# Performance work log

Measured on AMD Instinct MI355X. Metric: run time of the kernel, lower is better.

Reference implementation:

```python
import jax, jax.numpy as jnp
import numpy as np

R = 64          # plane_resolution
C = 32          # plane_channels
H = 128         # mlp_hidden
FEAT = 3 * C


def _grid_sample_bilinear(plane, coords):
    # plane: [C, R, R]; coords: [M, 2] normalized to [-1, 1], (x->W, y->H)
    # align_corners=True, padding_mode='border'
    r = plane.shape[-1]
    ix = (coords[:, 0] + 1.0) * 0.5 * (r - 1)
    iy = (coords[:, 1] + 1.0) * 0.5 * (r - 1)
    ix = jnp.clip(ix, 0.0, r - 1.0)
    iy = jnp.clip(iy, 0.0, r - 1.0)
    x0 = jnp.floor(ix).astype(jnp.int32)
    y0 = jnp.floor(iy).astype(jnp.int32)
    x1 = jnp.minimum(x0 + 1, r - 1)
    y1 = jnp.minimum(y0 + 1, r - 1)
    wx = ix - x0.astype(ix.dtype)
    wy = iy - y0.astype(iy.dtype)
    v00 = plane[:, y0, x0]  # [C, M]
    v01 = plane[:, y0, x1]
    v10 = plane[:, y1, x0]
    v11 = plane[:, y1, x1]
    out = (v00 * (1 - wx) * (1 - wy) + v01 * wx * (1 - wy)
           + v10 * (1 - wx) * wy + v11 * wx * wy)
    return out.T  # [M, C]


def setup_inputs() -> dict:
    key = jax.random.key(0)
    ks = jax.random.split(key, 12)
    B, N = 4, 262144
    points = jax.random.uniform(ks[0], (B, N, 3), dtype=jnp.float32)  # in [0,1) subset of [-1,1]
    planes = jax.random.normal(ks[1], (3, C, R, R), dtype=jnp.float32) * 0.01
    def lin(k, fan_in, fan_out):
        kw, kb = jax.random.split(k)
        bound = 1.0 / np.sqrt(fan_in)
        W = jax.random.uniform(kw, (fan_out, fan_in), jnp.float32, -bound, bound)
        b = jax.random.uniform(kb, (fan_out,), jnp.float32, -bound, bound)
        return W, b
    dW1, db1 = lin(ks[2], FEAT, H)
    dW2, db2 = lin(ks[3], H, H)
    dW3, db3 = lin(ks[4], H, 1)
    rW1, rb1 = lin(ks[5], FEAT, H)
    rW2, rb2 = lin(ks[6], H, 3)
    return dict(points=points, planes=planes,
                dW1=dW1, db1=db1, dW2=dW2, db2=db2, dW3=dW3, db3=db3,
                rW1=rW1, rb1=rb1, rW2=rW2, rb2=rb2)


def reference(points, planes, dW1, db1, dW2, db2, dW3, db3, rW1, rb1, rW2, rb2):
    B, N, _ = points.shape
    p = points.reshape(B * N, 3)
    x, y, z = p[:, 0], p[:, 1], p[:, 2]
    # coords for xy, xz, yz planes: [3, M, 2]
    coords = jnp.stack([jnp.stack([x, y], -1),
                        jnp.stack([x, z], -1),
                        jnp.stack([y, z], -1)], 0)
    feats = jax.vmap(_grid_sample_bilinear)(planes, coords)  # [3, M, C]
    feat = jnp.concatenate([feats[0], feats[1], feats[2]], axis=-1)  # [M, 3C]
    h = jax.nn.relu(feat @ dW1.T + db1)
    h = jax.nn.relu(h @ dW2.T + db2)
    density = jax.nn.softplus(h @ dW3.T + db3)  # [M, 1]
    r = jax.nn.relu(feat @ rW1.T + rb1)
    rgb = jax.nn.sigmoid(r @ rW2.T + rb2)  # [M, 3]
    return rgb.reshape(B, N, 3), density.reshape(B, N, 1)
```

## Files before the change

kernel.cpp:

```cpp
#include <hip/hip_runtime.h>
#include <hip/hip_bf16.h>
#include <math.h>

#define RR 64
#define CC 32
#define NPTS (4*262144)

typedef __attribute__((ext_vector_type(8))) short short8;
typedef __attribute__((ext_vector_type(4))) float f32x4;
typedef __attribute__((ext_vector_type(4))) unsigned int u32x4;

static __device__ inline ushort f2bf(float x) {
    return __builtin_bit_cast(ushort, __float2bfloat16(x));
}
static __device__ inline uint32_t pk2(float a, float b) {
    return (uint32_t)f2bf(a) | ((uint32_t)f2bf(b) << 16);
}
static __device__ inline float relu(float x) { return fmaxf(x, 0.0f); }


__global__ void prepass(const float* __restrict__ planes,
                        const float* __restrict__ dW1, const float* __restrict__ rW1,
                        const float* __restrict__ dW2,
                        const float* __restrict__ db1, const float* __restrict__ rb1,
                        const float* __restrict__ db2, const float* __restrict__ dW3,
                        const float* __restrict__ rW2,
                        float* __restrict__ ws) {
    int tid = blockIdx.x * blockDim.x + threadIdx.x;
    ushort* W1T = (ushort*)(ws + 393216);
    ushort* W2T = W1T + 24576;
    float*  CWS = ws + 393216 + 20480;

    if (tid < 3 * CC * RR * RR) {
        int x = tid % RR, y = (tid / RR) % RR, ch = (tid / (RR * RR)) % CC, p = tid / (CC * RR * RR);
        ws[((p * RR + y) * RR + x) * CC + ch] = planes[tid];
    }
    if (tid < 24576) {
        int e = tid & 7, l = (tid >> 3) & 63, rem = tid >> 9;
        int p = rem % 3, nt = rem / 3;
        int j = nt * 16 + (l & 15);
        int k = p * 32 + (l >> 4) * 8 + e;
        float v = (j < 128) ? dW1[j * 96 + k] : rW1[(j - 128) * 96 + k];
        W1T[tid] = f2bf(v);
    }
    if (tid < 16384) {
        int e = tid & 7, l = (tid >> 3) & 63, rem = tid >> 9;
        int kt2 = rem & 3, nt2 = rem >> 2;
        int j2 = nt2 * 16 + (l & 15);
        int k = kt2 * 32 + (l >> 4) * 8 + e;
        W2T[tid] = f2bf(dW2[j2 * 128 + k]);
    }
    if (tid < 256) CWS[tid]       = (tid < 128) ? db1[tid] : rb1[tid - 128];
    if (tid < 128) CWS[256 + tid] = db2[tid];
    if (tid < 128) CWS[384 + tid] = dW3[tid];
    if (tid < 384) CWS[512 + tid] = rW2[tid];
}

static __device__ inline short8 sample_frag(const float* __restrict__ P,
                                            int plane_base, float cx, float cy, int g8) {
    float ix = (cx + 1.0f) * 31.5f; ix = fminf(fmaxf(ix, 0.0f), 63.0f);
    float iy = (cy + 1.0f) * 31.5f; iy = fminf(fmaxf(iy, 0.0f), 63.0f);
    int x0 = (int)ix, y0 = (int)iy;
    int x1 = min(x0 + 1, 63), y1 = min(y0 + 1, 63);
    float wx = ix - (float)x0, wy = iy - (float)y0;
    float w00 = (1.0f - wx) * (1.0f - wy), w01 = wx * (1.0f - wy);
    float w10 = (1.0f - wx) * wy,          w11 = wx * wy;
    int b00 = plane_base + (y0 * 64 + x0) * 32 + g8;
    int b01 = plane_base + (y0 * 64 + x1) * 32 + g8;
    int b10 = plane_base + (y1 * 64 + x0) * 32 + g8;
    int b11 = plane_base + (y1 * 64 + x1) * 32 + g8;
    f32x4 a0 = *(const f32x4*)(P + b00), a1 = *(const f32x4*)(P + b00 + 4);
    f32x4 c0 = *(const f32x4*)(P + b01), c1 = *(const f32x4*)(P + b01 + 4);
    f32x4 d0 = *(const f32x4*)(P + b10), d1 = *(const f32x4*)(P + b10 + 4);
    f32x4 e0 = *(const f32x4*)(P + b11), e1 = *(const f32x4*)(P + b11 + 4);
    float f0 = w00 * a0[0] + w01 * c0[0] + w10 * d0[0] + w11 * e0[0];
    float f1 = w00 * a0[1] + w01 * c0[1] + w10 * d0[1] + w11 * e0[1];
    float f2 = w00 * a0[2] + w01 * c0[2] + w10 * d0[2] + w11 * e0[2];
    float f3 = w00 * a0[3] + w01 * c0[3] + w10 * d0[3] + w11 * e0[3];
    float f4 = w00 * a1[0] + w01 * c1[0] + w10 * d1[0] + w11 * e1[0];
    float f5 = w00 * a1[1] + w01 * c1[1] + w10 * d1[1] + w11 * e1[1];
    float f6 = w00 * a1[2] + w01 * c1[2] + w10 * d1[2] + w11 * e1[2];
    float f7 = w00 * a1[3] + w01 * c1[3] + w10 * d1[3] + w11 * e1[3];
    u32x4 uu;
    uu[0] = pk2(f0, f1); uu[1] = pk2(f2, f3);
    uu[2] = pk2(f4, f5); uu[3] = pk2(f6, f7);
    return __builtin_bit_cast(short8, uu);
}

#define MFMA(a, b, c) __builtin_amdgcn_mfma_f32_16x16x32_bf16((a), (b), (c), 0, 0, 0)

__global__ __launch_bounds__(512, 2)
void nerf_mfma(const float* __restrict__ points, const float* __restrict__ ws,
               const float* __restrict__ db3g, const float* __restrict__ rb2g,
               float* __restrict__ rgb_out, float* __restrict__ den_out) {
    __shared__ __align__(16) ushort SB[42752];
    __shared__ __align__(16) ushort Hs[8][32][136];

    const float* P = ws;
    int tid = threadIdx.x;

    {
        const u32x4* src = (const u32x4*)(ws + 393216);
        u32x4* dst = (u32x4*)SB;
        #pragma unroll 2
        for (int j = tid; j < 5344; j += 512) dst[j] = src[j];
    }
    __syncthreads();

    const ushort* W1L = SB;
    const ushort* W2L = SB + 24576;
    const float*  Cl  = (const float*)(SB + 40960);

    int wid = tid >> 6, lane = tid & 63;
    int c = lane & 15, g = lane >> 4;
    int g8 = 8 * g;
    ushort (*H)[136] = Hs[wid];
    int gw = blockIdx.x * 8 + wid;

    float b3 = db3g[0];
    float rb0 = rb2g[0], rb1v = rb2g[1], rb2v = rb2g[2];

    for (int it = 0; it < 2; ++it) {
        int pbase = (gw * 2 + it) * 32;

        int ptA = pbase + c, ptB = pbase + c + 16;
        float xa = points[ptA * 3 + 0], ya = points[ptA * 3 + 1], za = points[ptA * 3 + 2];
        float xb = points[ptB * 3 + 0], yb = points[ptB * 3 + 1], zb = points[ptB * 3 + 2];
        short8 bfA0 = sample_frag(P, 0,      xa, ya, g8);
        short8 bfA1 = sample_frag(P, 131072, xa, za, g8);
        short8 bfA2 = sample_frag(P, 262144, ya, za, g8);
        short8 bfB0 = sample_frag(P, 0,      xb, yb, g8);
        short8 bfB1 = sample_frag(P, 131072, xb, zb, g8);
        short8 bfB2 = sample_frag(P, 262144, yb, zb, g8);

        #pragma unroll 4
        for (int nt = 0; nt < 8; ++nt) {
            const ushort* wp = W1L + nt * 1536 + lane * 8;
            short8 a0 = *(const short8*)(wp);
            short8 a1 = *(const short8*)(wp + 512);
            short8 a2 = *(const short8*)(wp + 1024);
            f32x4 accA = {0.f,0.f,0.f,0.f}, accB = {0.f,0.f,0.f,0.f};
            accA = MFMA(a0, bfA0, accA); accB = MFMA(a0, bfB0, accB);
            accA = MFMA(a1, bfA1, accA); accB = MFMA(a1, bfB1, accB);
            accA = MFMA(a2, bfA2, accA); accB = MFMA(a2, bfB2, accB);
            f32x4 bb = *(const f32x4*)(Cl + nt * 16 + 4 * g);
            uint2 wA, wB;
            wA.x = pk2(relu(accA[0] + bb[0]), relu(accA[1] + bb[1]));
            wA.y = pk2(relu(accA[2] + bb[2]), relu(accA[3] + bb[3]));
            wB.x = pk2(relu(accB[0] + bb[0]), relu(accB[1] + bb[1]));
            wB.y = pk2(relu(accB[2] + bb[2]), relu(accB[3] + bb[3]));
            *(uint2*)(&H[c][16 * nt + 4 * g])      = wA;
            *(uint2*)(&H[c + 16][16 * nt + 4 * g]) = wB;
        }

        float racc0A = 0.f, racc0B = 0.f, racc1A = 0.f, racc1B = 0.f, racc2A = 0.f, racc2B = 0.f;
        #pragma unroll 4
        for (int nt = 8; nt < 16; ++nt) {
            const ushort* wp = W1L + nt * 1536 + lane * 8;
            short8 a0 = *(const short8*)(wp);
            short8 a1 = *(const short8*)(wp + 512);
            short8 a2 = *(const short8*)(wp + 1024);
            f32x4 accA = {0.f,0.f,0.f,0.f}, accB = {0.f,0.f,0.f,0.f};
            accA = MFMA(a0, bfA0, accA); accB = MFMA(a0, bfB0, accB);
            accA = MFMA(a1, bfA1, accA); accB = MFMA(a1, bfB1, accB);
            accA = MFMA(a2, bfA2, accA); accB = MFMA(a2, bfB2, accB);
            int jo = (nt - 8) * 16 + 4 * g;
            f32x4 bb = *(const f32x4*)(Cl + 128 + jo);
            f32x4 w0 = *(const f32x4*)(Cl + 512 + jo);
            f32x4 w1 = *(const f32x4*)(Cl + 640 + jo);
            f32x4 w2 = *(const f32x4*)(Cl + 768 + jo);
            #pragma unroll
            for (int r = 0; r < 4; ++r) {
                float vA = relu(accA[r] + bb[r]);
                float vB = relu(accB[r] + bb[r]);
                racc0A = fmaf(w0[r], vA, racc0A); racc0B = fmaf(w0[r], vB, racc0B);
                racc1A = fmaf(w1[r], vA, racc1A); racc1B = fmaf(w1[r], vB, racc1B);
                racc2A = fmaf(w2[r], vA, racc2A); racc2B = fmaf(w2[r], vB, racc2B);
            }
        }

        asm volatile("s_waitcnt lgkmcnt(0)" ::: "memory");
        __builtin_amdgcn_sched_barrier(0);

        short8 b2A0 = *(const short8*)(&H[c][g8]);
        short8 b2A1 = *(const short8*)(&H[c][32 + g8]);
        short8 b2A2 = *(const short8*)(&H[c][64 + g8]);
        short8 b2A3 = *(const short8*)(&H[c][96 + g8]);
        short8 b2B0 = *(const short8*)(&H[c + 16][g8]);
        short8 b2B1 = *(const short8*)(&H[c + 16][32 + g8]);
        short8 b2B2 = *(const short8*)(&H[c + 16][64 + g8]);
        short8 b2B3 = *(const short8*)(&H[c + 16][96 + g8]);

        float daccA = 0.f, daccB = 0.f;
        #pragma unroll 2
        for (int nt2 = 0; nt2 < 8; ++nt2) {
            const ushort* wp = W2L + nt2 * 2048 + lane * 8;
            short8 a0 = *(const short8*)(wp);
            short8 a1 = *(const short8*)(wp + 512);
            short8 a2 = *(const short8*)(wp + 1024);
            short8 a3 = *(const short8*)(wp + 1536);
            f32x4 accA = {0.f,0.f,0.f,0.f}, accB = {0.f,0.f,0.f,0.f};
            accA = MFMA(a0, b2A0, accA); accB = MFMA(a0, b2B0, accB);
            accA = MFMA(a1, b2A1, accA); accB = MFMA(a1, b2B1, accB);
            accA = MFMA(a2, b2A2, accA); accB = MFMA(a2, b2B2, accB);
            accA = MFMA(a3, b2A3, accA); accB = MFMA(a3, b2B3, accB);
            f32x4 bb = *(const f32x4*)(Cl + 256 + nt2 * 16 + 4 * g);
            f32x4 w3 = *(const f32x4*)(Cl + 384 + nt2 * 16 + 4 * g);
            #pragma unroll
            for (int r = 0; r < 4; ++r) {
                daccA = fmaf(w3[r], relu(accA[r] + bb[r]), daccA);
                daccB = fmaf(w3[r], relu(accB[r] + bb[r]), daccB);
            }
        }

        {
            float v = daccA; v += __shfl_xor(v, 16, 64); v += __shfl_xor(v, 32, 64); v += b3;
            float sp = fmaxf(v, 0.0f) + log1pf(expf(-fabsf(v)));
            if (g == 0) den_out[pbase + c] = sp;
        }
        {
            float v = daccB; v += __shfl_xor(v, 16, 64); v += __shfl_xor(v, 32, 64); v += b3;
            float sp = fmaxf(v, 0.0f) + log1pf(expf(-fabsf(v)));
            if (g == 0) den_out[pbase + 16 + c] = sp;
        }
        {
            float v = racc0A; v += __shfl_xor(v, 16, 64); v += __shfl_xor(v, 32, 64); v += rb0;
            if (g == 0) rgb_out[(pbase + c) * 3 + 0] = 1.0f / (1.0f + expf(-v));
        }
        {
            float v = racc1A; v += __shfl_xor(v, 16, 64); v += __shfl_xor(v, 32, 64); v += rb1v;
            if (g == 0) rgb_out[(pbase + c) * 3 + 1] = 1.0f / (1.0f + expf(-v));
        }
        {
            float v = racc2A; v += __shfl_xor(v, 16, 64); v += __shfl_xor(v, 32, 64); v += rb2v;
            if (g == 0) rgb_out[(pbase + c) * 3 + 2] = 1.0f / (1.0f + expf(-v));
        }
        {
            float v = racc0B; v += __shfl_xor(v, 16, 64); v += __shfl_xor(v, 32, 64); v += rb0;
            if (g == 0) rgb_out[(pbase + 16 + c) * 3 + 0] = 1.0f / (1.0f + expf(-v));
        }
        {
            float v = racc1B; v += __shfl_xor(v, 16, 64); v += __shfl_xor(v, 32, 64); v += rb1v;
            if (g == 0) rgb_out[(pbase + 16 + c) * 3 + 1] = 1.0f / (1.0f + expf(-v));
        }
        {
            float v = racc2B; v += __shfl_xor(v, 16, 64); v += __shfl_xor(v, 32, 64); v += rb2v;
            if (g == 0) rgb_out[(pbase + 16 + c) * 3 + 2] = 1.0f / (1.0f + expf(-v));
        }

        asm volatile("" ::: "memory");
    }
}

extern "C" void kernel_launch(void* const* d_in, const int* in_sizes, int n_in,
                              void* d_out, int out_size, void* d_ws, size_t ws_size,
                              hipStream_t stream) {
    const float* points = (const float*)d_in[0];
    const float* planes = (const float*)d_in[1];
    const float* dW1    = (const float*)d_in[2];
    const float* db1    = (const float*)d_in[3];
    const float* dW2    = (const float*)d_in[4];
    const float* db2    = (const float*)d_in[5];
    const float* dW3    = (const float*)d_in[6];
    const float* db3    = (const float*)d_in[7];
    const float* rW1    = (const float*)d_in[8];
    const float* rb1    = (const float*)d_in[9];
    const float* rW2    = (const float*)d_in[10];
    const float* rb2    = (const float*)d_in[11];

    float* out     = (float*)d_out;
    float* rgb_out = out;
    float* den_out = out + 3 * NPTS;
    float* ws      = (float*)d_ws;

    prepass<<<1536, 256, 0, stream>>>(planes, dW1, rW1, dW2, db1, rb1,
                                      db2, dW3, rW2, ws);
    nerf_mfma<<<2048, 512, 0, stream>>>(points, ws, db3, rb2, rgb_out, den_out);
}
```

Measured before the change: 235.4 us.

## Transpose MLP hidden activations via lane shuffles and run rgb head on MFMA

The per-wave LDS staging buffer for layer-1 outputs is removed. Accumulator fragments are now rearranged into B-operand fragments for the next matmul with cross-lane shuffles, which drops LDS writes, reads and the waitcnt barrier. The rgb head's 128x3 projection moves from scalar FMAs plus shuffle reductions to a padded bf16 MFMA, with rW2 pre-packed in the prepass. Freeing the LDS allows 1024-thread blocks at higher occupancy, at the cost of many shuffle instructions, register pressure under launch_bounds(1024,4), and bf16 rounding of the rgb head inputs.

```diff
diff --git a/kernel.cpp b/kernel.cpp
--- a/kernel.cpp
+++ b/kernel.cpp
@@ -29,7 +29,8 @@
     int tid = blockIdx.x * blockDim.x + threadIdx.x;
     ushort* W1T = (ushort*)(ws + 393216);
     ushort* W2T = W1T + 24576;
-    float*  CWS = ws + 393216 + 20480;
+    ushort* RWT = W2T + 16384;
+    float*  CWS = (float*)(RWT + 2048);
 
     if (tid < 3 * CC * RR * RR) {
         int x = tid % RR, y = (tid / RR) % RR, ch = (tid / (RR * RR)) % CC, p = tid / (CC * RR * RR);
@@ -50,10 +51,14 @@
         int k = kt2 * 32 + (l >> 4) * 8 + e;
         W2T[tid] = f2bf(dW2[j2 * 128 + k]);
     }
+    if (tid < 2048) {
+        int e = tid & 7, l = (tid >> 3) & 63, kt2 = tid >> 9;
+        int cc = l & 15, gg = l >> 4;
+        RWT[tid] = (cc < 3) ? f2bf(rW2[cc * 128 + kt2 * 32 + gg * 8 + e]) : (ushort)0;
+    }
     if (tid < 256) CWS[tid]       = (tid < 128) ? db1[tid] : rb1[tid - 128];
     if (tid < 128) CWS[256 + tid] = db2[tid];
     if (tid < 128) CWS[384 + tid] = dW3[tid];
-    if (tid < 384) CWS[512 + tid] = rW2[tid];
 }
 
 static __device__ inline short8 sample_frag(const float* __restrict__ P,
@@ -89,12 +94,36 @@
 
 #define MFMA(a, b, c) __builtin_amdgcn_mfma_f32_16x16x32_bf16((a), (b), (c), 0, 0, 0)
 
-__global__ __launch_bounds__(512, 2)
+#define L1NT(nt, oA0, oA1, oB0, oB1) { \
+    const ushort* wp_ = W1L + (nt) * 1536 + lane * 8; \
+    short8 a0_ = *(const short8*)(wp_); \
+    short8 a1_ = *(const short8*)(wp_ + 512); \
+    short8 a2_ = *(const short8*)(wp_ + 1024); \
+    f32x4 accA_ = {0.f,0.f,0.f,0.f}, accB_ = {0.f,0.f,0.f,0.f}; \
+    accA_ = MFMA(a0_, bfA0, accA_); accB_ = MFMA(a0_, bfB0, accB_); \
+    accA_ = MFMA(a1_, bfA1, accA_); accB_ = MFMA(a1_, bfB1, accB_); \
+    accA_ = MFMA(a2_, bfA2, accA_); accB_ = MFMA(a2_, bfB2, accB_); \
+    f32x4 bb_ = *(const f32x4*)(Cl + (nt) * 16 + 4 * g); \
+    oA0 = pk2(relu(accA_[0] + bb_[0]), relu(accA_[1] + bb_[1])); \
+    oA1 = pk2(relu(accA_[2] + bb_[2]), relu(accA_[3] + bb_[3])); \
+    oB0 = pk2(relu(accB_[0] + bb_[0]), relu(accB_[1] + bb_[1])); \
+    oB1 = pk2(relu(accB_[2] + bb_[2]), relu(accB_[3] + bb_[3])); }
+
+#define TRKT(p0a, p0b, p1a, p1b, outf) { \
+    unsigned lo0_ = __shfl(p0a, s0, 64), hi0_ = __shfl(p1a, s0, 64); \
+    unsigned lo1_ = __shfl(p0b, s0, 64), hi1_ = __shfl(p1b, s0, 64); \
+    unsigned lo2_ = __shfl(p0a, s1, 64), hi2_ = __shfl(p1a, s1, 64); \
+    unsigned lo3_ = __shfl(p0b, s1, 64), hi3_ = __shfl(p1b, s1, 64); \
+    u32x4 uu_; \
+    uu_[0] = gh ? hi0_ : lo0_;  uu_[1] = gh ? hi1_ : lo1_; \
+    uu_[2] = gh ? hi2_ : lo2_;  uu_[3] = gh ? hi3_ : lo3_; \
+    outf = __builtin_bit_cast(short8, uu_); }
+
+__global__ __launch_bounds__(1024, 4)
 void nerf_mfma(const float* __restrict__ points, const float* __restrict__ ws,
                const float* __restrict__ db3g, const float* __restrict__ rb2g,
                float* __restrict__ rgb_out, float* __restrict__ den_out) {
-    __shared__ __align__(16) ushort SB[42752];
-    __shared__ __align__(16) ushort Hs[8][32][136];
+    __shared__ __align__(16) ushort SB[44032];
 
     const float* P = ws;
     int tid = threadIdx.x;
@@ -102,22 +131,24 @@
     {
         const u32x4* src = (const u32x4*)(ws + 393216);
         u32x4* dst = (u32x4*)SB;
-        #pragma unroll 2
-        for (int j = tid; j < 5344; j += 512) dst[j] = src[j];
+        for (int j = tid; j < 5504; j += 1024) dst[j] = src[j];
     }
     __syncthreads();
 
     const ushort* W1L = SB;
     const ushort* W2L = SB + 24576;
-    const float*  Cl  = (const float*)(SB + 40960);
+    const ushort* RWL = SB + 40960;
+    const float*  Cl  = (const float*)(SB + 43008);
 
     int wid = tid >> 6, lane = tid & 63;
     int c = lane & 15, g = lane >> 4;
     int g8 = 8 * g;
-    ushort (*H)[136] = Hs[wid];
-    int gw = blockIdx.x * 8 + wid;
-
-    float b3 = db3g[0];
+    int s0 = c + ((g & 1) << 5);
+    int s1 = s0 + 16;
+    bool gh = (g >= 2);
+    int gw = blockIdx.x * 16 + wid;
+
+    float b3  = db3g[0];
     float rb0 = rb2g[0], rb1v = rb2g[1], rb2v = rb2g[2];
 
     for (int it = 0; it < 2; ++it) {
@@ -133,63 +164,29 @@
         short8 bfB1 = sample_frag(P, 131072, xb, zb, g8);
         short8 bfB2 = sample_frag(P, 262144, yb, zb, g8);
 
-        #pragma unroll 4
-        for (int nt = 0; nt < 8; ++nt) {
-            const ushort* wp = W1L + nt * 1536 + lane * 8;
-            short8 a0 = *(const short8*)(wp);
-            short8 a1 = *(const short8*)(wp + 512);
-            short8 a2 = *(const short8*)(wp + 1024);
-            f32x4 accA = {0.f,0.f,0.f,0.f}, accB = {0.f,0.f,0.f,0.f};
-            accA = MFMA(a0, bfA0, accA); accB = MFMA(a0, bfB0, accB);
-            accA = MFMA(a1, bfA1, accA); accB = MFMA(a1, bfB1, accB);
-            accA = MFMA(a2, bfA2, accA); accB = MFMA(a2, bfB2, accB);
-            f32x4 bb = *(const f32x4*)(Cl + nt * 16 + 4 * g);
-            uint2 wA, wB;
-            wA.x = pk2(relu(accA[0] + bb[0]), relu(accA[1] + bb[1]));
-            wA.y = pk2(relu(accA[2] + bb[2]), relu(accA[3] + bb[3]));
-            wB.x = pk2(relu(accB[0] + bb[0]), relu(accB[1] + bb[1]));
-            wB.y = pk2(relu(accB[2] + bb[2]), relu(accB[3] + bb[3]));
-            *(uint2*)(&H[c][16 * nt + 4 * g])      = wA;
-            *(uint2*)(&H[c + 16][16 * nt + 4 * g]) = wB;
-        }
-
-        float racc0A = 0.f, racc0B = 0.f, racc1A = 0.f, racc1B = 0.f, racc2A = 0.f, racc2B = 0.f;
-        #pragma unroll 4
-        for (int nt = 8; nt < 16; ++nt) {
-            const ushort* wp = W1L + nt * 1536 + lane * 8;
-            short8 a0 = *(const short8*)(wp);
-            short8 a1 = *(const short8*)(wp + 512);
-            short8 a2 = *(const short8*)(wp + 1024);
-            f32x4 accA = {0.f,0.f,0.f,0.f}, accB = {0.f,0.f,0.f,0.f};
-            accA = MFMA(a0, bfA0, accA); accB = MFMA(a0, bfB0, accB);
-            accA = MFMA(a1, bfA1, accA); accB = MFMA(a1, bfB1, accB);
-            accA = MFMA(a2, bfA2, accA); accB = MFMA(a2, bfB2, accB);
-            int jo = (nt - 8) * 16 + 4 * g;
-            f32x4 bb = *(const f32x4*)(Cl + 128 + jo);
-            f32x4 w0 = *(const f32x4*)(Cl + 512 + jo);
-            f32x4 w1 = *(const f32x4*)(Cl + 640 + jo);
-            f32x4 w2 = *(const f32x4*)(Cl + 768 + jo);
-            #pragma unroll
-            for (int r = 0; r < 4; ++r) {
-                float vA = relu(accA[r] + bb[r]);
-                float vB = relu(accB[r] + bb[r]);
-                racc0A = fmaf(w0[r], vA, racc0A); racc0B = fmaf(w0[r], vB, racc0B);
-                racc1A = fmaf(w1[r], vA, racc1A); racc1B = fmaf(w1[r], vB, racc1B);
-                racc2A = fmaf(w2[r], vA, racc2A); racc2B = fmaf(w2[r], vB, racc2B);
-            }
-        }
-
-        asm volatile("s_waitcnt lgkmcnt(0)" ::: "memory");
-        __builtin_amdgcn_sched_barrier(0);
-
-        short8 b2A0 = *(const short8*)(&H[c][g8]);
-        short8 b2A1 = *(const short8*)(&H[c][32 + g8]);
-        short8 b2A2 = *(const short8*)(&H[c][64 + g8]);
-        short8 b2A3 = *(const short8*)(&H[c][96 + g8]);
-        short8 b2B0 = *(const short8*)(&H[c + 16][g8]);
-        short8 b2B1 = *(const short8*)(&H[c + 16][32 + g8]);
-        short8 b2B2 = *(const short8*)(&H[c + 16][64 + g8]);
-        short8 b2B3 = *(const short8*)(&H[c + 16][96 + g8]);
+        unsigned pA0, pA1, qA0, qA1, pB0, pB1, qB0, qB1;
+
+        f32x4 rAacc = {0.f,0.f,0.f,0.f}, rBacc = {0.f,0.f,0.f,0.f};
+        #define RKT(kt2) { \
+            L1NT(8 + 2*(kt2), pA0, pA1, pB0, pB1); \
+            L1NT(9 + 2*(kt2), qA0, qA1, qB0, qB1); \
+            short8 brA_, brB_; \
+            TRKT(pA0, pA1, qA0, qA1, brA_); \
+            TRKT(pB0, pB1, qB0, qB1, brB_); \
+            short8 aw_ = *(const short8*)(RWL + (kt2) * 512 + lane * 8); \
+            rAacc = MFMA(aw_, brA_, rAacc); \
+            rBacc = MFMA(aw_, brB_, rBacc); }
+        RKT(0) RKT(1) RKT(2) RKT(3)
+        #undef RKT
+
+        short8 b2A0, b2A1, b2A2, b2A3, b2B0, b2B1, b2B2, b2B3;
+        #define DKT(kt2, B2A, B2B) { \
+            L1NT(2*(kt2),     pA0, pA1, pB0, pB1); \
+            L1NT(2*(kt2) + 1, qA0, qA1, qB0, qB1); \
+            TRKT(pA0, pA1, qA0, qA1, B2A); \
+            TRKT(pB0, pB1, qB0, qB1, B2B); }
+        DKT(0, b2A0, b2B0) DKT(1, b2A1, b2B1) DKT(2, b2A2, b2B2) DKT(3, b2A3, b2B3)
+        #undef DKT
 
         float daccA = 0.f, daccB = 0.f;
         #pragma unroll 2
@@ -223,32 +220,14 @@
             float sp = fmaxf(v, 0.0f) + log1pf(expf(-fabsf(v)));
             if (g == 0) den_out[pbase + 16 + c] = sp;
         }
-        {
-            float v = racc0A; v += __shfl_xor(v, 16, 64); v += __shfl_xor(v, 32, 64); v += rb0;
-            if (g == 0) rgb_out[(pbase + c) * 3 + 0] = 1.0f / (1.0f + expf(-v));
-        }
-        {
-            float v = racc1A; v += __shfl_xor(v, 16, 64); v += __shfl_xor(v, 32, 64); v += rb1v;
-            if (g == 0) rgb_out[(pbase + c) * 3 + 1] = 1.0f / (1.0f + expf(-v));
-        }
-        {
-            float v = racc2A; v += __shfl_xor(v, 16, 64); v += __shfl_xor(v, 32, 64); v += rb2v;
-            if (g == 0) rgb_out[(pbase + c) * 3 + 2] = 1.0f / (1.0f + expf(-v));
-        }
-        {
-            float v = racc0B; v += __shfl_xor(v, 16, 64); v += __shfl_xor(v, 32, 64); v += rb0;
-            if (g == 0) rgb_out[(pbase + 16 + c) * 3 + 0] = 1.0f / (1.0f + expf(-v));
-        }
-        {
-            float v = racc1B; v += __shfl_xor(v, 16, 64); v += __shfl_xor(v, 32, 64); v += rb1v;
-            if (g == 0) rgb_out[(pbase + 16 + c) * 3 + 1] = 1.0f / (1.0f + expf(-v));
-        }
-        {
-            float v = racc2B; v += __shfl_xor(v, 16, 64); v += __shfl_xor(v, 32, 64); v += rb2v;
-            if (g == 0) rgb_out[(pbase + 16 + c) * 3 + 2] = 1.0f / (1.0f + expf(-v));
-        }
-
-        asm volatile("" ::: "memory");
+        if (g == 0) {
+            rgb_out[ptA * 3 + 0] = 1.0f / (1.0f + expf(-(rAacc[0] + rb0)));
+            rgb_out[ptA * 3 + 1] = 1.0f / (1.0f + expf(-(rAacc[1] + rb1v)));
+            rgb_out[ptA * 3 + 2] = 1.0f / (1.0f + expf(-(rAacc[2] + rb2v)));
+            rgb_out[ptB * 3 + 0] = 1.0f / (1.0f + expf(-(rBacc[0] + rb0)));
+            rgb_out[ptB * 3 + 1] = 1.0f / (1.0f + expf(-(rBacc[1] + rb1v)));
+            rgb_out[ptB * 3 + 2] = 1.0f / (1.0f + expf(-(rBacc[2] + rb2v)));
+        }
     }
 }
 
@@ -275,5 +254,5 @@
 
     prepass<<<1536, 256, 0, stream>>>(planes, dW1, rW1, dW2, db1, rb1,
                                       db2, dW3, rW2, ws);
-    nerf_mfma<<<2048, 512, 0, stream>>>(points, ws, db3, rb2, rgb_out, den_out);
-}
+    nerf_mfma<<<1024, 1024, 0, stream>>>(points, ws, db3, rb2, rgb_out, den_out);
+}
```

Measured after the change: 886.7 us. 3.77x slower.

## Use 1024-thread blocks with one 16-point tile per wave iteration

Applied to the files above, without the earlier changes.

Each wave now processes one 16-point MFMA column tile per iteration (four iterations) instead of two interleaved 16-point tiles, and blocks grow to 16 waves with launch bounds (1024,1). This lowers register pressure per wave and halves the per-wave H staging buffer, while the per-block weight copy into LDS is amortized over more waves. The cost is less MFMA interleaving to hide latency, since each weight fragment loaded from LDS is now reused for one tile instead of two, and one block per CU gives less block-level overlap.

```diff
diff --git a/kernel.cpp b/kernel.cpp
--- a/kernel.cpp
+++ b/kernel.cpp
@@ -89,12 +89,12 @@
 
 #define MFMA(a, b, c) __builtin_amdgcn_mfma_f32_16x16x32_bf16((a), (b), (c), 0, 0, 0)
 
-__global__ __launch_bounds__(512, 2)
+__global__ __launch_bounds__(1024, 1)
 void nerf_mfma(const float* __restrict__ points, const float* __restrict__ ws,
                const float* __restrict__ db3g, const float* __restrict__ rb2g,
                float* __restrict__ rgb_out, float* __restrict__ den_out) {
     __shared__ __align__(16) ushort SB[42752];
-    __shared__ __align__(16) ushort Hs[8][32][136];
+    __shared__ __align__(16) ushort Hs[16][16][136];
 
     const float* P = ws;
     int tid = threadIdx.x;
@@ -102,8 +102,7 @@
     {
         const u32x4* src = (const u32x4*)(ws + 393216);
         u32x4* dst = (u32x4*)SB;
-        #pragma unroll 2
-        for (int j = tid; j < 5344; j += 512) dst[j] = src[j];
+        for (int j = tid; j < 5344; j += 1024) dst[j] = src[j];
     }
     __syncthreads();
 
@@ -115,23 +114,19 @@
     int c = lane & 15, g = lane >> 4;
     int g8 = 8 * g;
     ushort (*H)[136] = Hs[wid];
-    int gw = blockIdx.x * 8 + wid;
-
-    float b3 = db3g[0];
+    int gw = blockIdx.x * 16 + wid;
+
+    float b3  = db3g[0];
     float rb0 = rb2g[0], rb1v = rb2g[1], rb2v = rb2g[2];
 
-    for (int it = 0; it < 2; ++it) {
-        int pbase = (gw * 2 + it) * 32;
-
-        int ptA = pbase + c, ptB = pbase + c + 16;
+    for (int it = 0; it < 4; ++it) {
+        int pbase = (gw * 4 + it) * 16;
+
+        int ptA = pbase + c;
         float xa = points[ptA * 3 + 0], ya = points[ptA * 3 + 1], za = points[ptA * 3 + 2];
-        float xb = points[ptB * 3 + 0], yb = points[ptB * 3 + 1], zb = points[ptB * 3 + 2];
         short8 bfA0 = sample_frag(P, 0,      xa, ya, g8);
         short8 bfA1 = sample_frag(P, 131072, xa, za, g8);
         short8 bfA2 = sample_frag(P, 262144, ya, za, g8);
-        short8 bfB0 = sample_frag(P, 0,      xb, yb, g8);
-        short8 bfB1 = sample_frag(P, 131072, xb, zb, g8);
-        short8 bfB2 = sample_frag(P, 262144, yb, zb, g8);
 
         #pragma unroll 4
         for (int nt = 0; nt < 8; ++nt) {
@@ -139,31 +134,28 @@
             short8 a0 = *(const short8*)(wp);
             short8 a1 = *(const short8*)(wp + 512);
             short8 a2 = *(const short8*)(wp + 1024);
-            f32x4 accA = {0.f,0.f,0.f,0.f}, accB = {0.f,0.f,0.f,0.f};
-            accA = MFMA(a0, bfA0, accA); accB = MFMA(a0, bfB0, accB);
-            accA = MFMA(a1, bfA1, accA); accB = MFMA(a1, bfB1, accB);
-            accA = MFMA(a2, bfA2, accA); accB = MFMA(a2, bfB2, accB);
+            f32x4 accA = {0.f,0.f,0.f,0.f};
+            accA = MFMA(a0, bfA0, accA);
+            accA = MFMA(a1, bfA1, accA);
+            accA = MFMA(a2, bfA2, accA);
             f32x4 bb = *(const f32x4*)(Cl + nt * 16 + 4 * g);
-            uint2 wA, wB;
+            uint2 wA;
             wA.x = pk2(relu(accA[0] + bb[0]), relu(accA[1] + bb[1]));
             wA.y = pk2(relu(accA[2] + bb[2]), relu(accA[3] + bb[3]));
-            wB.x = pk2(relu(accB[0] + bb[0]), relu(accB[1] + bb[1]));
-            wB.y = pk2(relu(accB[2] + bb[2]), relu(accB[3] + bb[3]));
-            *(uint2*)(&H[c][16 * nt + 4 * g])      = wA;
-            *(uint2*)(&H[c + 16][16 * nt + 4 * g]) = wB;
-        }
-
-        float racc0A = 0.f, racc0B = 0.f, racc1A = 0.f, racc1B = 0.f, racc2A = 0.f, racc2B = 0.f;
+            *(uint2*)(&H[c][16 * nt + 4 * g]) = wA;
+        }
+
+        float racc0A = 0.f, racc1A = 0.f, racc2A = 0.f;
         #pragma unroll 4
         for (int nt = 8; nt < 16; ++nt) {
             const ushort* wp = W1L + nt * 1536 + lane * 8;
             short8 a0 = *(const short8*)(wp);
             short8 a1 = *(const short8*)(wp + 512);
             short8 a2 = *(const short8*)(wp + 1024);
-            f32x4 accA = {0.f,0.f,0.f,0.f}, accB = {0.f,0.f,0.f,0.f};
-            accA = MFMA(a0, bfA0, accA); accB = MFMA(a0, bfB0, accB);
-            accA = MFMA(a1, bfA1, accA); accB = MFMA(a1, bfB1, accB);
-            accA = MFMA(a2, bfA2, accA); accB = MFMA(a2, bfB2, accB);
+            f32x4 accA = {0.f,0.f,0.f,0.f};
+            accA = MFMA(a0, bfA0, accA);
+            accA = MFMA(a1, bfA1, accA);
+            accA = MFMA(a2, bfA2, accA);
             int jo = (nt - 8) * 16 + 4 * g;
             f32x4 bb = *(const f32x4*)(Cl + 128 + jo);
             f32x4 w0 = *(const f32x4*)(Cl + 512 + jo);
@@ -172,10 +164,9 @@
             #pragma unroll
             for (int r = 0; r < 4; ++r) {
                 float vA = relu(accA[r] + bb[r]);
-                float vB = relu(accB[r] + bb[r]);
-                racc0A = fmaf(w0[r], vA, racc0A); racc0B = fmaf(w0[r], vB, racc0B);
-                racc1A = fmaf(w1[r], vA, racc1A); racc1B = fmaf(w1[r], vB, racc1B);
-                racc2A = fmaf(w2[r], vA, racc2A); racc2B = fmaf(w2[r], vB, racc2B);
+                racc0A = fmaf(w0[r], vA, racc0A);
+                racc1A = fmaf(w1[r], vA, racc1A);
+                racc2A = fmaf(w2[r], vA, racc2A);
             }
         }
 
@@ -186,12 +177,8 @@
         short8 b2A1 = *(const short8*)(&H[c][32 + g8]);
         short8 b2A2 = *(const short8*)(&H[c][64 + g8]);
         short8 b2A3 = *(const short8*)(&H[c][96 + g8]);
-        short8 b2B0 = *(const short8*)(&H[c + 16][g8]);
-        short8 b2B1 = *(const short8*)(&H[c + 16][32 + g8]);
-        short8 b2B2 = *(const short8*)(&H[c + 16][64 + g8]);
-        short8 b2B3 = *(const short8*)(&H[c + 16][96 + g8]);
-
-        float daccA = 0.f, daccB = 0.f;
+
+        float daccA = 0.f;
         #pragma unroll 2
         for (int nt2 = 0; nt2 < 8; ++nt2) {
             const ushort* wp = W2L + nt2 * 2048 + lane * 8;
@@ -199,53 +186,34 @@
             short8 a1 = *(const short8*)(wp + 512);
             short8 a2 = *(const short8*)(wp + 1024);
             short8 a3 = *(const short8*)(wp + 1536);
-            f32x4 accA = {0.f,0.f,0.f,0.f}, accB = {0.f,0.f,0.f,0.f};
-            accA = MFMA(a0, b2A0, accA); accB = MFMA(a0, b2B0, accB);
-            accA = MFMA(a1, b2A1, accA); accB = MFMA(a1, b2B1, accB);
-            accA = MFMA(a2, b2A2, accA); accB = MFMA(a2, b2B2, accB);
-            accA = MFMA(a3, b2A3, accA); accB = MFMA(a3, b2B3, accB);
+            f32x4 accA = {0.f,0.f,0.f,0.f};
+            accA = MFMA(a0, b2A0, accA);
+            accA = MFMA(a1, b2A1, accA);
+            accA = MFMA(a2, b2A2, accA);
+            accA = MFMA(a3, b2A3, accA);
             f32x4 bb = *(const f32x4*)(Cl + 256 + nt2 * 16 + 4 * g);
             f32x4 w3 = *(const f32x4*)(Cl + 384 + nt2 * 16 + 4 * g);
             #pragma unroll
-            for (int r = 0; r < 4; ++r) {
+            for (int r = 0; r < 4; ++r)
                 daccA = fmaf(w3[r], relu(accA[r] + bb[r]), daccA);
-                daccB = fmaf(w3[r], relu(accB[r] + bb[r]), daccB);
-            }
         }
 
         {
             float v = daccA; v += __shfl_xor(v, 16, 64); v += __shfl_xor(v, 32, 64); v += b3;
             float sp = fmaxf(v, 0.0f) + log1pf(expf(-fabsf(v)));
-            if (g == 0) den_out[pbase + c] = sp;
-        }
-        {
-            float v = daccB; v += __shfl_xor(v, 16, 64); v += __shfl_xor(v, 32, 64); v += b3;
-            float sp = fmaxf(v, 0.0f) + log1pf(expf(-fabsf(v)));
-            if (g == 0) den_out[pbase + 16 + c] = sp;
+            if (g == 0) den_out[ptA] = sp;
         }
         {
             float v = racc0A; v += __shfl_xor(v, 16, 64); v += __shfl_xor(v, 32, 64); v += rb0;
-            if (g == 0) rgb_out[(pbase + c) * 3 + 0] = 1.0f / (1.0f + expf(-v));
+            if (g == 0) rgb_out[ptA * 3 + 0] = 1.0f / (1.0f + expf(-v));
         }
         {
             float v = racc1A; v += __shfl_xor(v, 16, 64); v += __shfl_xor(v, 32, 64); v += rb1v;
-            if (g == 0) rgb_out[(pbase + c) * 3 + 1] = 1.0f / (1.0f + expf(-v));
+            if (g == 0) rgb_out[ptA * 3 + 1] = 1.0f / (1.0f + expf(-v));
         }
         {
             float v = racc2A; v += __shfl_xor(v, 16, 64); v += __shfl_xor(v, 32, 64); v += rb2v;
-            if (g == 0) rgb_out[(pbase + c) * 3 + 2] = 1.0f / (1.0f + expf(-v));
-        }
-        {
-            float v = racc0B; v += __shfl_xor(v, 16, 64); v += __shfl_xor(v, 32, 64); v += rb0;
-            if (g == 0) rgb_out[(pbase + 16 + c) * 3 + 0] = 1.0f / (1.0f + expf(-v));
-        }
-        {
-            float v = racc1B; v += __shfl_xor(v, 16, 64); v += __shfl_xor(v, 32, 64); v += rb1v;
-            if (g == 0) rgb_out[(pbase + 16 + c) * 3 + 1] = 1.0f / (1.0f + expf(-v));
-        }
-        {
-            float v = racc2B; v += __shfl_xor(v, 16, 64); v += __shfl_xor(v, 32, 64); v += rb2v;
-            if (g == 0) rgb_out[(pbase + 16 + c) * 3 + 2] = 1.0f / (1.0f + expf(-v));
+            if (g == 0) rgb_out[ptA * 3 + 2] = 1.0f / (1.0f + expf(-v));
         }
 
         asm volatile("" ::: "memory");
@@ -275,5 +243,5 @@
 
     prepass<<<1536, 256, 0, stream>>>(planes, dW1, rW1, dW2, db1, rb1,
                                       db2, dW3, rW2, ws);
-    nerf_mfma<<<2048, 512, 0, stream>>>(points, ws, db3, rb2, rgb_out, den_out);
-}
+    nerf_mfma<<<1024, 1024, 0, stream>>>(points, ws, db3, rb2, rgb_out, den_out);
+}
```

After: 224.0 us. 4.8% less time.

## Use 1024-thread blocks with halved per-wave hidden buffer and earlier rgb output

Applied to the files above, without the earlier changes.

Blocks grow to 16 waves (1024 threads, one block per CU in launch bounds) and the grid halves, so the shared weight copy into LDS is amortized over twice as many waves. The per-wave H staging buffer shrinks to 16 rows: point A's hidden activations are written and read back first, while point B's are held packed in registers and written into the same buffer afterwards. The rgb head is reduced and stored right after its layer, before the density layer, to shorten live ranges. In exchange the kernel carries more VGPR pressure and extra LDS fences, and the launch-bounds change may alter register allocation and occupancy.

```diff
diff --git a/kernel.cpp b/kernel.cpp
--- a/kernel.cpp
+++ b/kernel.cpp
@@ -89,12 +89,36 @@
 
 #define MFMA(a, b, c) __builtin_amdgcn_mfma_f32_16x16x32_bf16((a), (b), (c), 0, 0, 0)
 
-__global__ __launch_bounds__(512, 2)
+#define DNT(nt, HB0, HB1) { \
+    const ushort* wp_ = W1L + (nt) * 1536 + lane * 8; \
+    short8 a0_ = *(const short8*)(wp_); \
+    short8 a1_ = *(const short8*)(wp_ + 512); \
+    short8 a2_ = *(const short8*)(wp_ + 1024); \
+    f32x4 accA_ = {0.f,0.f,0.f,0.f}, accB_ = {0.f,0.f,0.f,0.f}; \
+    accA_ = MFMA(a0_, bfA0, accA_); accB_ = MFMA(a0_, bfB0, accB_); \
+    accA_ = MFMA(a1_, bfA1, accA_); accB_ = MFMA(a1_, bfB1, accB_); \
+    accA_ = MFMA(a2_, bfA2, accA_); accB_ = MFMA(a2_, bfB2, accB_); \
+    f32x4 bb_ = *(const f32x4*)(Cl + (nt) * 16 + 4 * g); \
+    uint2 wA_; \
+    wA_.x = pk2(relu(accA_[0] + bb_[0]), relu(accA_[1] + bb_[1])); \
+    wA_.y = pk2(relu(accA_[2] + bb_[2]), relu(accA_[3] + bb_[3])); \
+    *(uint2*)(&H[c][16 * (nt) + 4 * g]) = wA_; \
+    HB0 = pk2(relu(accB_[0] + bb_[0]), relu(accB_[1] + bb_[1])); \
+    HB1 = pk2(relu(accB_[2] + bb_[2]), relu(accB_[3] + bb_[3])); }
+
+#define HWB(nt, HB0, HB1) { \
+    uint2 t_; t_.x = HB0; t_.y = HB1; \
+    *(uint2*)(&H[c][16 * (nt) + 4 * g]) = t_; }
+
+#define LDSFENCE { asm volatile("s_waitcnt lgkmcnt(0)" ::: "memory"); \
+                   __builtin_amdgcn_sched_barrier(0); }
+
+__global__ __launch_bounds__(1024, 1)
 void nerf_mfma(const float* __restrict__ points, const float* __restrict__ ws,
                const float* __restrict__ db3g, const float* __restrict__ rb2g,
                float* __restrict__ rgb_out, float* __restrict__ den_out) {
     __shared__ __align__(16) ushort SB[42752];
-    __shared__ __align__(16) ushort Hs[8][32][136];
+    __shared__ __align__(16) ushort Hs[16][16][136];
 
     const float* P = ws;
     int tid = threadIdx.x;
@@ -102,8 +126,7 @@
     {
         const u32x4* src = (const u32x4*)(ws + 393216);
         u32x4* dst = (u32x4*)SB;
-        #pragma unroll 2
-        for (int j = tid; j < 5344; j += 512) dst[j] = src[j];
+        for (int j = tid; j < 5344; j += 1024) dst[j] = src[j];
     }
     __syncthreads();
 
@@ -115,9 +138,9 @@
     int c = lane & 15, g = lane >> 4;
     int g8 = 8 * g;
     ushort (*H)[136] = Hs[wid];
-    int gw = blockIdx.x * 8 + wid;
-
-    float b3 = db3g[0];
+    int gw = blockIdx.x * 16 + wid;
+
+    float b3  = db3g[0];
     float rb0 = rb2g[0], rb1v = rb2g[1], rb2v = rb2g[2];
 
     for (int it = 0; it < 2; ++it) {
@@ -133,27 +156,7 @@
         short8 bfB1 = sample_frag(P, 131072, xb, zb, g8);
         short8 bfB2 = sample_frag(P, 262144, yb, zb, g8);
 
-        #pragma unroll 4
-        for (int nt = 0; nt < 8; ++nt) {
-            const ushort* wp = W1L + nt * 1536 + lane * 8;
-            short8 a0 = *(const short8*)(wp);
-            short8 a1 = *(const short8*)(wp + 512);
-            short8 a2 = *(const short8*)(wp + 1024);
-            f32x4 accA = {0.f,0.f,0.f,0.f}, accB = {0.f,0.f,0.f,0.f};
-            accA = MFMA(a0, bfA0, accA); accB = MFMA(a0, bfB0, accB);
-            accA = MFMA(a1, bfA1, accA); accB = MFMA(a1, bfB1, accB);
-            accA = MFMA(a2, bfA2, accA); accB = MFMA(a2, bfB2, accB);
-            f32x4 bb = *(const f32x4*)(Cl + nt * 16 + 4 * g);
-            uint2 wA, wB;
-            wA.x = pk2(relu(accA[0] + bb[0]), relu(accA[1] + bb[1]));
-            wA.y = pk2(relu(accA[2] + bb[2]), relu(accA[3] + bb[3]));
-            wB.x = pk2(relu(accB[0] + bb[0]), relu(accB[1] + bb[1]));
-            wB.y = pk2(relu(accB[2] + bb[2]), relu(accB[3] + bb[3]));
-            *(uint2*)(&H[c][16 * nt + 4 * g])      = wA;
-            *(uint2*)(&H[c + 16][16 * nt + 4 * g]) = wB;
-        }
-
-        float racc0A = 0.f, racc0B = 0.f, racc1A = 0.f, racc1B = 0.f, racc2A = 0.f, racc2B = 0.f;
+        float r0A = 0.f, r1A = 0.f, r2A = 0.f, r0B = 0.f, r1B = 0.f, r2B = 0.f;
         #pragma unroll 4
         for (int nt = 8; nt < 16; ++nt) {
             const ushort* wp = W1L + nt * 1536 + lane * 8;
@@ -173,23 +176,52 @@
             for (int r = 0; r < 4; ++r) {
                 float vA = relu(accA[r] + bb[r]);
                 float vB = relu(accB[r] + bb[r]);
-                racc0A = fmaf(w0[r], vA, racc0A); racc0B = fmaf(w0[r], vB, racc0B);
-                racc1A = fmaf(w1[r], vA, racc1A); racc1B = fmaf(w1[r], vB, racc1B);
-                racc2A = fmaf(w2[r], vA, racc2A); racc2B = fmaf(w2[r], vB, racc2B);
-            }
-        }
-
-        asm volatile("s_waitcnt lgkmcnt(0)" ::: "memory");
-        __builtin_amdgcn_sched_barrier(0);
-
+                r0A = fmaf(w0[r], vA, r0A); r0B = fmaf(w0[r], vB, r0B);
+                r1A = fmaf(w1[r], vA, r1A); r1B = fmaf(w1[r], vB, r1B);
+                r2A = fmaf(w2[r], vA, r2A); r2B = fmaf(w2[r], vB, r2B);
+            }
+        }
+        {
+            float v0 = r0A, v1 = r1A, v2 = r2A;
+            v0 += __shfl_xor(v0, 16, 64); v0 += __shfl_xor(v0, 32, 64);
+            v1 += __shfl_xor(v1, 16, 64); v1 += __shfl_xor(v1, 32, 64);
+            v2 += __shfl_xor(v2, 16, 64); v2 += __shfl_xor(v2, 32, 64);
+            if (g == 0) {
+                rgb_out[ptA * 3 + 0] = 1.0f / (1.0f + expf(-(v0 + rb0)));
+                rgb_out[ptA * 3 + 1] = 1.0f / (1.0f + expf(-(v1 + rb1v)));
+                rgb_out[ptA * 3 + 2] = 1.0f / (1.0f + expf(-(v2 + rb2v)));
+            }
+        }
+        {
+            float v0 = r0B, v1 = r1B, v2 = r2B;
+            v0 += __shfl_xor(v0, 16, 64); v0 += __shfl_xor(v0, 32, 64);
+            v1 += __shfl_xor(v1, 16, 64); v1 += __shfl_xor(v1, 32, 64);
+            v2 += __shfl_xor(v2, 16, 64); v2 += __shfl_xor(v2, 32, 64);
+            if (g == 0) {
+                rgb_out[ptB * 3 + 0] = 1.0f / (1.0f + expf(-(v0 + rb0)));
+                rgb_out[ptB * 3 + 1] = 1.0f / (1.0f + expf(-(v1 + rb1v)));
+                rgb_out[ptB * 3 + 2] = 1.0f / (1.0f + expf(-(v2 + rb2v)));
+            }
+        }
+
+        unsigned hB0a, hB0b, hB1a, hB1b, hB2a, hB2b, hB3a, hB3b;
+        unsigned hB4a, hB4b, hB5a, hB5b, hB6a, hB6b, hB7a, hB7b;
+        DNT(0, hB0a, hB0b) DNT(1, hB1a, hB1b) DNT(2, hB2a, hB2b) DNT(3, hB3a, hB3b)
+        DNT(4, hB4a, hB4b) DNT(5, hB5a, hB5b) DNT(6, hB6a, hB6b) DNT(7, hB7a, hB7b)
+
+        LDSFENCE
         short8 b2A0 = *(const short8*)(&H[c][g8]);
         short8 b2A1 = *(const short8*)(&H[c][32 + g8]);
         short8 b2A2 = *(const short8*)(&H[c][64 + g8]);
         short8 b2A3 = *(const short8*)(&H[c][96 + g8]);
-        short8 b2B0 = *(const short8*)(&H[c + 16][g8]);
-        short8 b2B1 = *(const short8*)(&H[c + 16][32 + g8]);
-        short8 b2B2 = *(const short8*)(&H[c + 16][64 + g8]);
-        short8 b2B3 = *(const short8*)(&H[c + 16][96 + g8]);
+        LDSFENCE
+        HWB(0, hB0a, hB0b) HWB(1, hB1a, hB1b) HWB(2, hB2a, hB2b) HWB(3, hB3a, hB3b)
+        HWB(4, hB4a, hB4b) HWB(5, hB5a, hB5b) HWB(6, hB6a, hB6b) HWB(7, hB7a, hB7b)
+        LDSFENCE
+        short8 b2B0 = *(const short8*)(&H[c][g8]);
+        short8 b2B1 = *(const short8*)(&H[c][32 + g8]);
+        short8 b2B2 = *(const short8*)(&H[c][64 + g8]);
+        short8 b2B3 = *(const short8*)(&H[c][96 + g8]);
 
         float daccA = 0.f, daccB = 0.f;
         #pragma unroll 2
@@ -216,36 +248,12 @@
         {
             float v = daccA; v += __shfl_xor(v, 16, 64); v += __shfl_xor(v, 32, 64); v += b3;
             float sp = fmaxf(v, 0.0f) + log1pf(expf(-fabsf(v)));
-            if (g == 0) den_out[pbase + c] = sp;
+            if (g == 0) den_out[ptA] = sp;
         }
         {
             float v = daccB; v += __shfl_xor(v, 16, 64); v += __shfl_xor(v, 32, 64); v += b3;
             float sp = fmaxf(v, 0.0f) + log1pf(expf(-fabsf(v)));
-            if (g == 0) den_out[pbase + 16 + c] = sp;
-        }
-        {
-            float v = racc0A; v += __shfl_xor(v, 16, 64); v += __shfl_xor(v, 32, 64); v += rb0;
-            if (g == 0) rgb_out[(pbase + c) * 3 + 0] = 1.0f / (1.0f + expf(-v));
-        }
-        {
-            float v = racc1A; v += __shfl_xor(v, 16, 64); v += __shfl_xor(v, 32, 64); v += rb1v;
-            if (g == 0) rgb_out[(pbase + c) * 3 + 1] = 1.0f / (1.0f + expf(-v));
-        }
-        {
-            float v = racc2A; v += __shfl_xor(v, 16, 64); v += __shfl_xor(v, 32, 64); v += rb2v;
-            if (g == 0) rgb_out[(pbase + c) * 3 + 2] = 1.0f / (1.0f + expf(-v));
-        }
-        {
-            float v = racc0B; v += __shfl_xor(v, 16, 64); v += __shfl_xor(v, 32, 64); v += rb0;
-            if (g == 0) rgb_out[(pbase + 16 + c) * 3 + 0] = 1.0f / (1.0f + expf(-v));
-        }
-        {
-            float v = racc1B; v += __shfl_xor(v, 16, 64); v += __shfl_xor(v, 32, 64); v += rb1v;
-            if (g == 0) rgb_out[(pbase + 16 + c) * 3 + 1] = 1.0f / (1.0f + expf(-v));
-        }
-        {
-            float v = racc2B; v += __shfl_xor(v, 16, 64); v += __shfl_xor(v, 32, 64); v += rb2v;
-            if (g == 0) rgb_out[(pbase + 16 + c) * 3 + 2] = 1.0f / (1.0f + expf(-v));
+            if (g == 0) den_out[ptB] = sp;
         }
 
         asm volatile("" ::: "memory");
@@ -275,5 +283,5 @@
 
     prepass<<<1536, 256, 0, stream>>>(planes, dW1, rW1, dW2, db1, rb1,
                                       db2, dW3, rW2, ws);
-    nerf_mfma<<<2048, 512, 0, stream>>>(points, ws, db3, rb2, rgb_out, den_out);
-}
+    nerf_mfma<<<1024, 1024, 0, stream>>>(points, ws, db3, rb2, rgb_out, den_out);
+}
```

New measurement: 228.8 us. 2.8% less time.
